# Performance work log

Measured on AMD Instinct MI355X. Metric: run time of the kernel, lower is better.

## Reference

```python
import jax, jax.numpy as jnp
import numpy as np

OUT = 2048        # weight_size[0]
IN_BASE = 2048    # original input features
N_EMBED = 64      # replacements per iteration
IN_TOT = IN_BASE + 2 * N_EMBED  # 2176, weight_size[1]
NNZ_W = 400000
NNZ_B = 1024
BATCH = 8192


def setup_inputs() -> dict:
    key = jax.random.key(0)
    ks = jax.random.split(key, 10)
    return {
        "x": jax.random.normal(ks[0], (BATCH, IN_BASE), dtype=jnp.float32),
        "weight_vals": jax.random.normal(ks[1], (NNZ_W,), dtype=jnp.float32),
        "weight_rows": jax.random.randint(ks[2], (NNZ_W,), 0, OUT, dtype=jnp.int32),
        "weight_cols": jax.random.randint(ks[3], (NNZ_W,), 0, IN_TOT, dtype=jnp.int32),
        "bias_vals": jax.random.normal(ks[4], (NNZ_B,), dtype=jnp.float32),
        "bias_idx": jax.random.randint(ks[5], (NNZ_B,), 0, OUT, dtype=jnp.int32),
        "embed0_vals": jax.random.uniform(ks[6], (N_EMBED,), dtype=jnp.float32),
        "embed0_parents": jax.random.randint(ks[7], (N_EMBED,), 0, IN_BASE, dtype=jnp.int32),
        "embed1_vals": jax.random.uniform(ks[8], (N_EMBED,), dtype=jnp.float32),
        "embed1_parents": jax.random.randint(ks[9], (N_EMBED,), 0, IN_BASE + N_EMBED, dtype=jnp.int32),
    }


def reference(x, weight_vals, weight_rows, weight_cols, bias_vals, bias_idx,
              embed0_vals, embed0_parents, embed1_vals, embed1_parents):
    # EmbedLinear layers: each appends one new feature per stored row,
    # new_feat[:, c] = value[c] * x[:, parent[c]]  (single nnz per sparse row)
    x = jnp.concatenate([x, x[:, embed0_parents] * embed0_vals[None, :]], axis=1)  # [B, 2112]
    x = jnp.concatenate([x, x[:, embed1_parents] * embed1_vals[None, :]], axis=1)  # [B, 2176]
    # sparse weight -> dense via scatter-add (coalesce semantics sum duplicates)
    W = jnp.zeros((OUT, IN_TOT), dtype=weight_vals.dtype).at[weight_rows, weight_cols].add(weight_vals)
    b = jnp.zeros((OUT,), dtype=bias_vals.dtype).at[bias_idx].add(bias_vals)
    # (W @ x^T)^T + b  ==  x @ W^T + b
    return x @ W.T + b[None, :]
```

## Files before the change

kernel.cpp:

```cpp
#include <hip/hip_runtime.h>
#include <stdint.h>

#define OUT_F   2048
#define IN_BASE 2048
#define N_EMB   64
#define IN_TOT  2176
#define NNZ_W   400000
#define NNZ_B   1024
#define BATCH   8192

typedef __bf16 bf16x8 __attribute__((ext_vector_type(8)));
typedef __bf16 bf16x4 __attribute__((ext_vector_type(4)));
typedef float  floatx16 __attribute__((ext_vector_type(16)));

__global__ void __launch_bounds__(256) build_x_kernel(
    const float* __restrict__ x,
    const float* __restrict__ e0v, const int* __restrict__ e0p,
    const float* __restrict__ e1v, const int* __restrict__ e1p,
    __bf16* __restrict__ xb)
{
    const int GROUPS = IN_TOT / 4;
    int gid = blockIdx.x * 256 + threadIdx.x;
    int b = gid / GROUPS;
    int g = gid - b * GROUPS;
    const float* xr = x + (size_t)b * IN_BASE;

    float v[4];
    if (g < IN_BASE / 4) {
        const float4 t = *(const float4*)(xr + g * 4);
        v[0] = t.x; v[1] = t.y; v[2] = t.z; v[3] = t.w;
    } else if (g < (IN_BASE + N_EMB) / 4) {
        int j = (g - IN_BASE / 4) * 4;
#pragma unroll
        for (int t = 0; t < 4; t++) v[t] = e0v[j + t] * xr[e0p[j + t]];
    } else {
        int j = (g - (IN_BASE + N_EMB) / 4) * 4;
#pragma unroll
        for (int t = 0; t < 4; t++) {
            int p = e1p[j + t];
            float base = (p < IN_BASE) ? xr[p]
                                       : e0v[p - IN_BASE] * xr[e0p[p - IN_BASE]];
            v[t] = e1v[j + t] * base;
        }
    }
    bf16x4 o;
    o[0] = (__bf16)v[0]; o[1] = (__bf16)v[1]; o[2] = (__bf16)v[2]; o[3] = (__bf16)v[3];
    *(bf16x4*)(xb + (size_t)b * IN_TOT + g * 4) = o;
}

__global__ void __launch_bounds__(256) scatter_kernel(
    const float* __restrict__ wv, const int* __restrict__ wr,
    const int* __restrict__ wc,
    const float* __restrict__ bv, const int* __restrict__ bi,
    float* __restrict__ Wf, float* __restrict__ bf)
{
    int i = blockIdx.x * 256 + threadIdx.x;
    if (i < NNZ_W) {
        atomicAdd(Wf + (size_t)wr[i] * IN_TOT + wc[i], wv[i]);
    } else if (i < NNZ_W + NNZ_B) {
        int j = i - NNZ_W;
        atomicAdd(bf + bi[j], bv[j]);
    }
}

__global__ void __launch_bounds__(256) w_to_bf16_kernel(
    const float* __restrict__ Wf, __bf16* __restrict__ Wb)
{
    int e = (blockIdx.x * 256 + threadIdx.x) * 4;
    const float4 t = *(const float4*)(Wf + e);
    bf16x4 o;
    o[0] = (__bf16)t.x; o[1] = (__bf16)t.y; o[2] = (__bf16)t.z; o[3] = (__bf16)t.w;
    *(bf16x4*)(Wb + e) = o;
}

#define BM 128
#define BN 128
#define BK 64

__global__ void __launch_bounds__(256) gemm_kernel(
    const __bf16* __restrict__ A,
    const __bf16* __restrict__ W,
    const float*  __restrict__ bias,
    float* __restrict__ C)
{
    __shared__ __bf16 sA[BM * BK];
    __shared__ __bf16 sB[BN * BK];

    const int tid   = threadIdx.x;
    const int bm    = blockIdx.x;
    const int bn    = blockIdx.y;
    const int wave  = tid >> 6;
    const int lane  = tid & 63;
    const int wm    = (wave >> 1) * 64;
    const int wn    = (wave & 1) * 64;
    const int l32   = lane & 31;
    const int khalf = lane >> 5;

    floatx16 acc[2][2] = {};

    const int srow   = tid >> 3;
    const int kchunk = ((tid & 7) ^ ((tid >> 3) & 7)) * 8;
    const __bf16* Ag = A + (size_t)(bm * BM + srow) * IN_TOT + kchunk;
    const __bf16* Wg = W + (size_t)(bn * BN + srow) * IN_TOT + kchunk;
    char* sAb = (char*)sA;
    char* sBb = (char*)sB;

    for (int k0 = 0; k0 < IN_TOT; k0 += BK) {
#pragma unroll
        for (int i = 0; i < 4; i++) {
            __builtin_amdgcn_global_load_lds(
                (__attribute__((address_space(1))) void*)(uintptr_t)(Ag + (size_t)i * 32 * IN_TOT + k0),
                (__attribute__((address_space(3))) void*)(sAb + i * 4096 + tid * 16),
                16, 0, 0);
            __builtin_amdgcn_global_load_lds(
                (__attribute__((address_space(1))) void*)(uintptr_t)(Wg + (size_t)i * 32 * IN_TOT + k0),
                (__attribute__((address_space(3))) void*)(sBb + i * 4096 + tid * 16),
                16, 0, 0);
        }
        __syncthreads();

#pragma unroll
        for (int ks = 0; ks < 4; ks++) {
            const int sl = ((ks * 2 + khalf) ^ (l32 & 7)) * 8;
            bf16x8 af[2], bfr[2];
#pragma unroll
            for (int mi = 0; mi < 2; mi++)
                af[mi] = *(const bf16x8*)(sA + (wm + mi * 32 + l32) * BK + sl);
#pragma unroll
            for (int ni = 0; ni < 2; ni++)
                bfr[ni] = *(const bf16x8*)(sB + (wn + ni * 32 + l32) * BK + sl);
#pragma unroll
            for (int mi = 0; mi < 2; mi++)
#pragma unroll
                for (int ni = 0; ni < 2; ni++)
                    acc[mi][ni] = __builtin_amdgcn_mfma_f32_32x32x16_bf16(
                        af[mi], bfr[ni], acc[mi][ni], 0, 0, 0);
        }
        __syncthreads();
    }

#pragma unroll
    for (int mi = 0; mi < 2; mi++) {
#pragma unroll
        for (int ni = 0; ni < 2; ni++) {
            const int colg = bn * BN + wn + ni * 32 + l32;
            const float bv = bias[colg];
            const int rowb = bm * BM + wm + mi * 32 + 4 * khalf;
#pragma unroll
            for (int reg = 0; reg < 16; reg++) {
                const int rowg = rowb + (reg & 3) + 8 * (reg >> 2);
                C[(size_t)rowg * OUT_F + colg] = acc[mi][ni][reg] + bv;
            }
        }
    }
}

extern "C" void kernel_launch(void* const* d_in, const int* in_sizes, int n_in,
                              void* d_out, int out_size, void* d_ws, size_t ws_size,
                              hipStream_t stream) {
    const float* x      = (const float*)d_in[0];
    const float* w_vals = (const float*)d_in[1];
    const int*   w_rows = (const int*)  d_in[2];
    const int*   w_cols = (const int*)  d_in[3];
    const float* b_vals = (const float*)d_in[4];
    const int*   b_idx  = (const int*)  d_in[5];
    const float* e0v    = (const float*)d_in[6];
    const int*   e0p    = (const int*)  d_in[7];
    const float* e1v    = (const float*)d_in[8];
    const int*   e1p    = (const int*)  d_in[9];
    float* out = (float*)d_out;

    char* ws = (char*)d_ws;
    const size_t W_F32_BYTES  = (size_t)OUT_F * IN_TOT * 4;
    const size_t B_F32_BYTES  = (size_t)OUT_F * 4;
    const size_t W_BF16_BYTES = (size_t)OUT_F * IN_TOT * 2;
    float*  Wf = (float*)ws;
    float*  bf = (float*)(ws + W_F32_BYTES);
    __bf16* Wb = (__bf16*)(ws + W_F32_BYTES + B_F32_BYTES);
    __bf16* xb = (__bf16*)(ws + W_F32_BYTES + B_F32_BYTES + W_BF16_BYTES);

    hipMemsetAsync(Wf, 0, W_F32_BYTES + B_F32_BYTES, stream);

    build_x_kernel<<<(BATCH * (IN_TOT / 4)) / 256, 256, 0, stream>>>(
        x, e0v, e0p, e1v, e1p, xb);

    scatter_kernel<<<(NNZ_W + NNZ_B + 255) / 256, 256, 0, stream>>>(
        w_vals, w_rows, w_cols, b_vals, b_idx, Wf, bf);

    w_to_bf16_kernel<<<((size_t)OUT_F * IN_TOT / 4) / 256, 256, 0, stream>>>(Wf, Wb);

    dim3 grid(BATCH / BM, OUT_F / BN);
    gemm_kernel<<<grid, 256, 0, stream>>>(xb, Wb, bf, out);
}
```

Baseline: 248.3 us.

## Pre-pack operands into MFMA fragment layout and load directly to registers

Writes both the activation and weight matrices in a blocked layout that matches the 32x32x16 MFMA fragments, so each lane reads one contiguous 16-byte chunk per fragment. The GEMM then skips shared memory and barriers and streams fragments from global memory into registers with a two-stage software pipeline. The output tile grows to 128x256 per block, with each wave owning 64x128. This drops LDS traffic and synchronisation, but leaves operand reuse to L2/cache, and the larger accumulator set raises register pressure.

```diff
diff --git a/kernel.cpp b/kernel.cpp
--- a/kernel.cpp
+++ b/kernel.cpp
@@ -9,54 +9,87 @@
 #define NNZ_B   1024
 #define BATCH   8192
 
+#define KBLKS   (IN_TOT / 16)
+#define MBLKS   (BATCH / 32)
+#define NBLKS   (OUT_F / 32)
+
 typedef __bf16 bf16x8 __attribute__((ext_vector_type(8)));
 typedef __bf16 bf16x4 __attribute__((ext_vector_type(4)));
 typedef float  floatx16 __attribute__((ext_vector_type(16)));
 
-__global__ void __launch_bounds__(256) build_x_kernel(
+
+__global__ void __launch_bounds__(256) build_xt_kernel(
     const float* __restrict__ x,
     const float* __restrict__ e0v, const int* __restrict__ e0p,
     const float* __restrict__ e1v, const int* __restrict__ e1p,
-    __bf16* __restrict__ xb)
-{
-    const int GROUPS = IN_TOT / 4;
-    int gid = blockIdx.x * 256 + threadIdx.x;
-    int b = gid / GROUPS;
-    int g = gid - b * GROUPS;
-    const float* xr = x + (size_t)b * IN_BASE;
-
-    float v[4];
-    if (g < IN_BASE / 4) {
-        const float4 t = *(const float4*)(xr + g * 4);
-        v[0] = t.x; v[1] = t.y; v[2] = t.z; v[3] = t.w;
-    } else if (g < (IN_BASE + N_EMB) / 4) {
-        int j = (g - IN_BASE / 4) * 4;
-#pragma unroll
-        for (int t = 0; t < 4; t++) v[t] = e0v[j + t] * xr[e0p[j + t]];
-    } else {
-        int j = (g - (IN_BASE + N_EMB) / 4) * 4;
-#pragma unroll
-        for (int t = 0; t < 4; t++) {
-            int p = e1p[j + t];
-            float base = (p < IN_BASE) ? xr[p]
-                                       : e0v[p - IN_BASE] * xr[e0p[p - IN_BASE]];
-            v[t] = e1v[j + t] * base;
+    __bf16* __restrict__ A_t)
+{
+    __shared__ __bf16 tile[32 * 136];
+
+    const int t  = threadIdx.x;
+    const int mb = blockIdx.x;
+    const int c  = blockIdx.y;
+    const int m0 = mb * 32;
+
+    {
+        const int r  = t >> 3;
+        const int cc = t & 7;
+        __bf16* dst = tile + r * 136 + cc * 16;
+        if (c < 16) {
+            const float* src = x + (size_t)(m0 + r) * IN_BASE + c * 128 + cc * 16;
+#pragma unroll
+            for (int q = 0; q < 4; q++) {
+                float4 v = *(const float4*)(src + q * 4);
+                bf16x4 o;
+                o[0] = (__bf16)v.x; o[1] = (__bf16)v.y;
+                o[2] = (__bf16)v.z; o[3] = (__bf16)v.w;
+                *(bf16x4*)(dst + q * 4) = o;
+            }
+        } else {
+            const float* xr = x + (size_t)(m0 + r) * IN_BASE;
+#pragma unroll
+            for (int i = 0; i < 16; i++) {
+                int kk = cc * 16 + i;
+                float val;
+                if (kk < N_EMB) {
+                    val = e0v[kk] * xr[e0p[kk]];
+                } else {
+                    int j = kk - N_EMB;
+                    int p = e1p[j];
+                    float base = (p < IN_BASE) ? xr[p]
+                               : e0v[p - IN_BASE] * xr[e0p[p - IN_BASE]];
+                    val = e1v[j] * base;
+                }
+                dst[i] = (__bf16)val;
+            }
         }
     }
-    bf16x4 o;
-    o[0] = (__bf16)v[0]; o[1] = (__bf16)v[1]; o[2] = (__bf16)v[2]; o[3] = (__bf16)v[3];
-    *(bf16x4*)(xb + (size_t)b * IN_TOT + g * 4) = o;
+    __syncthreads();
+
+#pragma unroll
+    for (int g = 0; g < 2; g++) {
+        const int kbl  = g * 4 + (t >> 6);
+        const int lane = t & 63;
+        const int m    = lane & 31;
+        const int kh   = lane >> 5;
+        bf16x8 v = *(const bf16x8*)(tile + m * 136 + kbl * 16 + kh * 8);
+        const int kb = c * 8 + kbl;
+        *(bf16x8*)(A_t + ((size_t)kb * MBLKS + mb) * 512 + lane * 8) = v;
+    }
 }
 
 __global__ void __launch_bounds__(256) scatter_kernel(
     const float* __restrict__ wv, const int* __restrict__ wr,
     const int* __restrict__ wc,
     const float* __restrict__ bv, const int* __restrict__ bi,
-    float* __restrict__ Wf, float* __restrict__ bf)
+    float* __restrict__ Wf_t, float* __restrict__ bf)
 {
     int i = blockIdx.x * 256 + threadIdx.x;
     if (i < NNZ_W) {
-        atomicAdd(Wf + (size_t)wr[i] * IN_TOT + wc[i], wv[i]);
+        int r = wr[i], k = wc[i];
+        size_t idx = ((size_t)(k >> 4) * NBLKS + (r >> 5)) * 512
+                   + ((r & 31) + 32 * ((k >> 3) & 1)) * 8 + (k & 7);
+        atomicAdd(Wf_t + idx, wv[i]);
     } else if (i < NNZ_W + NNZ_B) {
         int j = i - NNZ_W;
         atomicAdd(bf + bi[j], bv[j]);
@@ -64,95 +97,87 @@
 }
 
 __global__ void __launch_bounds__(256) w_to_bf16_kernel(
-    const float* __restrict__ Wf, __bf16* __restrict__ Wb)
+    const float* __restrict__ Wf_t, __bf16* __restrict__ Wb_t)
 {
     int e = (blockIdx.x * 256 + threadIdx.x) * 4;
-    const float4 t = *(const float4*)(Wf + e);
+    const float4 v = *(const float4*)(Wf_t + e);
     bf16x4 o;
-    o[0] = (__bf16)t.x; o[1] = (__bf16)t.y; o[2] = (__bf16)t.z; o[3] = (__bf16)t.w;
-    *(bf16x4*)(Wb + e) = o;
-}
-
-#define BM 128
-#define BN 128
-#define BK 64
-
-__global__ void __launch_bounds__(256) gemm_kernel(
-    const __bf16* __restrict__ A,
-    const __bf16* __restrict__ W,
+    o[0] = (__bf16)v.x; o[1] = (__bf16)v.y; o[2] = (__bf16)v.z; o[3] = (__bf16)v.w;
+    *(bf16x4*)(Wb_t + e) = o;
+}
+
+__global__ void __launch_bounds__(256, 2) gemm_kernel(
+    const __bf16* __restrict__ A_t,
+    const __bf16* __restrict__ B_t,
     const float*  __restrict__ bias,
     float* __restrict__ C)
 {
-    __shared__ __bf16 sA[BM * BK];
-    __shared__ __bf16 sB[BN * BK];
-
-    const int tid   = threadIdx.x;
-    const int bm    = blockIdx.x;
-    const int bn    = blockIdx.y;
-    const int wave  = tid >> 6;
-    const int lane  = tid & 63;
-    const int wm    = (wave >> 1) * 64;
-    const int wn    = (wave & 1) * 64;
-    const int l32   = lane & 31;
-    const int khalf = lane >> 5;
-
-    floatx16 acc[2][2] = {};
-
-    const int srow   = tid >> 3;
-    const int kchunk = ((tid & 7) ^ ((tid >> 3) & 7)) * 8;
-    const __bf16* Ag = A + (size_t)(bm * BM + srow) * IN_TOT + kchunk;
-    const __bf16* Wg = W + (size_t)(bn * BN + srow) * IN_TOT + kchunk;
-    char* sAb = (char*)sA;
-    char* sBb = (char*)sB;
-
-    for (int k0 = 0; k0 < IN_TOT; k0 += BK) {
-#pragma unroll
-        for (int i = 0; i < 4; i++) {
-            __builtin_amdgcn_global_load_lds(
-                (__attribute__((address_space(1))) void*)(uintptr_t)(Ag + (size_t)i * 32 * IN_TOT + k0),
-                (__attribute__((address_space(3))) void*)(sAb + i * 4096 + tid * 16),
-                16, 0, 0);
-            __builtin_amdgcn_global_load_lds(
-                (__attribute__((address_space(1))) void*)(uintptr_t)(Wg + (size_t)i * 32 * IN_TOT + k0),
-                (__attribute__((address_space(3))) void*)(sBb + i * 4096 + tid * 16),
-                16, 0, 0);
-        }
-        __syncthreads();
-
-#pragma unroll
-        for (int ks = 0; ks < 4; ks++) {
-            const int sl = ((ks * 2 + khalf) ^ (l32 & 7)) * 8;
-            bf16x8 af[2], bfr[2];
-#pragma unroll
-            for (int mi = 0; mi < 2; mi++)
-                af[mi] = *(const bf16x8*)(sA + (wm + mi * 32 + l32) * BK + sl);
-#pragma unroll
-            for (int ni = 0; ni < 2; ni++)
-                bfr[ni] = *(const bf16x8*)(sB + (wn + ni * 32 + l32) * BK + sl);
-#pragma unroll
-            for (int mi = 0; mi < 2; mi++)
-#pragma unroll
-                for (int ni = 0; ni < 2; ni++)
-                    acc[mi][ni] = __builtin_amdgcn_mfma_f32_32x32x16_bf16(
-                        af[mi], bfr[ni], acc[mi][ni], 0, 0, 0);
-        }
-        __syncthreads();
-    }
-
+    const int tid  = threadIdx.x;
+    const int bn   = blockIdx.x & 7;
+    const int bm   = blockIdx.x >> 3;
+    const int wave = tid >> 6;
+    const int lane = tid & 63;
+    const int wr   = wave >> 1;
+    const int wc   = wave & 1;
+    const int mb0  = bm * 4 + wr * 2;
+    const int nb0  = bn * 8 + wc * 4;
+
+    const __bf16* Ap = A_t + ((size_t)mb0 * 64 + lane) * 8;
+    const __bf16* Bp = B_t + ((size_t)nb0 * 64 + lane) * 8;
+    const size_t AS = (size_t)MBLKS * 512;
+    const size_t BS = (size_t)NBLKS * 512;
+
+    floatx16 acc[2][4] = {};
+    bf16x8 a0[2], b0[4], a1[2], b1[4];
+
+#define LOADF(ar, br, kb)                                                     \
+    {                                                                         \
+        const __bf16* ap = Ap + (size_t)(kb) * AS;                            \
+        const __bf16* bp = Bp + (size_t)(kb) * BS;                            \
+        ar[0] = *(const bf16x8*)(ap);                                         \
+        ar[1] = *(const bf16x8*)(ap + 512);                                   \
+        br[0] = *(const bf16x8*)(bp);                                         \
+        br[1] = *(const bf16x8*)(bp + 512);                                   \
+        br[2] = *(const bf16x8*)(bp + 1024);                                  \
+        br[3] = *(const bf16x8*)(bp + 1536);                                  \
+    }
+#define MFMAF(ar, br)                                                         \
+    _Pragma("unroll")                                                         \
+    for (int mi = 0; mi < 2; mi++)                                            \
+        _Pragma("unroll")                                                     \
+        for (int ni = 0; ni < 4; ni++)                                        \
+            acc[mi][ni] = __builtin_amdgcn_mfma_f32_32x32x16_bf16(            \
+                ar[mi], br[ni], acc[mi][ni], 0, 0, 0);
+
+    LOADF(a0, b0, 0)
+    for (int i = 0; i < 67; i++) {
+        LOADF(a1, b1, 2 * i + 1)
+        MFMAF(a0, b0)
+        LOADF(a0, b0, 2 * i + 2)
+        MFMAF(a1, b1)
+    }
+    LOADF(a1, b1, 135)
+    MFMAF(a0, b0)
+    MFMAF(a1, b1)
+
+    const int l32 = lane & 31;
+    const int kh  = lane >> 5;
 #pragma unroll
     for (int mi = 0; mi < 2; mi++) {
-#pragma unroll
-        for (int ni = 0; ni < 2; ni++) {
-            const int colg = bn * BN + wn + ni * 32 + l32;
-            const float bv = bias[colg];
-            const int rowb = bm * BM + wm + mi * 32 + 4 * khalf;
+        const int rowb = bm * 128 + wr * 64 + mi * 32 + 4 * kh;
+#pragma unroll
+        for (int ni = 0; ni < 4; ni++) {
+            const int colg = bn * 256 + wc * 128 + ni * 32 + l32;
+            const float bvv = bias[colg];
 #pragma unroll
             for (int reg = 0; reg < 16; reg++) {
                 const int rowg = rowb + (reg & 3) + 8 * (reg >> 2);
-                C[(size_t)rowg * OUT_F + colg] = acc[mi][ni][reg] + bv;
+                C[(size_t)rowg * OUT_F + colg] = acc[mi][ni][reg] + bvv;
             }
         }
     }
+#undef LOADF
+#undef MFMAF
 }
 
 extern "C" void kernel_launch(void* const* d_in, const int* in_sizes, int n_in,
@@ -174,21 +199,20 @@
     const size_t W_F32_BYTES  = (size_t)OUT_F * IN_TOT * 4;
     const size_t B_F32_BYTES  = (size_t)OUT_F * 4;
     const size_t W_BF16_BYTES = (size_t)OUT_F * IN_TOT * 2;
-    float*  Wf = (float*)ws;
-    float*  bf = (float*)(ws + W_F32_BYTES);
-    __bf16* Wb = (__bf16*)(ws + W_F32_BYTES + B_F32_BYTES);
-    __bf16* xb = (__bf16*)(ws + W_F32_BYTES + B_F32_BYTES + W_BF16_BYTES);
-
-    hipMemsetAsync(Wf, 0, W_F32_BYTES + B_F32_BYTES, stream);
-
-    build_x_kernel<<<(BATCH * (IN_TOT / 4)) / 256, 256, 0, stream>>>(
-        x, e0v, e0p, e1v, e1p, xb);
+    float*  Wf_t = (float*)ws;
+    float*  bf   = (float*)(ws + W_F32_BYTES);
+    __bf16* Wb_t = (__bf16*)(ws + W_F32_BYTES + B_F32_BYTES);
+    __bf16* A_t  = (__bf16*)(ws + W_F32_BYTES + B_F32_BYTES + W_BF16_BYTES);
+
+    hipMemsetAsync(Wf_t, 0, W_F32_BYTES + B_F32_BYTES, stream);
+
+    dim3 bxg(MBLKS, 17);
+    build_xt_kernel<<<bxg, 256, 0, stream>>>(x, e0v, e0p, e1v, e1p, A_t);
 
     scatter_kernel<<<(NNZ_W + NNZ_B + 255) / 256, 256, 0, stream>>>(
-        w_vals, w_rows, w_cols, b_vals, b_idx, Wf, bf);
-
-    w_to_bf16_kernel<<<((size_t)OUT_F * IN_TOT / 4) / 256, 256, 0, stream>>>(Wf, Wb);
-
-    dim3 grid(BATCH / BM, OUT_F / BN);
-    gemm_kernel<<<grid, 256, 0, stream>>>(xb, Wb, bf, out);
-}
+        w_vals, w_rows, w_cols, b_vals, b_idx, Wf_t, bf);
+
+    w_to_bf16_kernel<<<((size_t)OUT_F * IN_TOT / 4) / 256, 256, 0, stream>>>(Wf_t, Wb_t);
+
+    gemm_kernel<<<512, 256, 0, stream>>>(A_t, Wb_t, bf, out);
+}
```

Measured after the change: 270.7 us. 1.09x slower.
